# Kernel optimization log

Hardware: AMD Instinct MI355X
Metric: run time of the kernel (lower is better)

The kernel has to match this reference:

```python
import jax, jax.numpy as jnp
import numpy as np

B, S, D, H = 2, 2048, 2048, 16
DH = D // H  # 128
MAX_SEQ = 2048


def _rope_tables(dim, max_seq_len):
    inv_freq = 1.0 / (10000.0 ** (jnp.arange(0, dim, 2, dtype=jnp.float32) / dim))
    t = jnp.arange(max_seq_len, dtype=jnp.float32)
    freqs = jnp.einsum('i,j->ij', t, inv_freq)          # [S, dim/2]
    emb = jnp.concatenate([freqs, freqs], axis=-1)       # [S, dim]
    return jnp.cos(emb), jnp.sin(emb)


def setup_inputs() -> dict:
    key = jax.random.key(0)
    kx, kq, kk, kv, ko = jax.random.split(key, 5)
    scale = 1.0 / np.sqrt(D)
    x = jax.random.normal(kx, (B, S, D), dtype=jnp.float32)
    # nn.Linear weights: [out_features, in_features], y = x @ W.T
    wq = jax.random.normal(kq, (H * DH, D), dtype=jnp.float32) * scale
    wk = jax.random.normal(kk, (H * DH, D), dtype=jnp.float32) * scale
    wv = jax.random.normal(kv, (H * DH, D), dtype=jnp.float32) * scale
    wo = jax.random.normal(ko, (D, H * DH), dtype=jnp.float32) * scale
    cos, sin = _rope_tables(DH, MAX_SEQ)
    return {"x": x, "wq": wq, "wk": wk, "wv": wv, "wo": wo,
            "cos": cos, "sin": sin}


def _rotate(t):
    # faithful to torch: cat([-t[..., 1::2], t[..., ::2]], dim=-1)
    return jnp.concatenate([-t[..., 1::2], t[..., ::2]], axis=-1)


def reference(x, wq, wk, wv, wo, cos, sin):
    b, s, _ = x.shape
    # QKV projections -> [b, h, s, dh]
    def proj(w):
        return jnp.einsum('bsd,ed->bse', x, w).reshape(b, s, H, DH).transpose(0, 2, 1, 3)
    q, k, v = proj(wq), proj(wk), proj(wv)
    c = cos[:s, :]  # [s, dh], broadcasts over b, h
    si = sin[:s, :]
    q = q * c + _rotate(q) * si
    k = k * c + _rotate(k) * si
    # scaled dot-product attention, non-causal
    scores = jnp.einsum('bhqd,bhkd->bhqk', q, k) / np.sqrt(DH)
    attn = jax.nn.softmax(scores, axis=-1)
    out = jnp.einsum('bhqk,bhkd->bhqd', attn, v)
    out = out.transpose(0, 2, 1, 3).reshape(b, s, H * DH)
    return jnp.einsum('bse,de->bsd', out, wo)
```

## Files before the change

### kernel.cpp

```cpp
#include <hip/hip_runtime.h>

#define SQ   2048
#define DIMD 2048
#define NH   16
#define HD   128
#define MR   4096
#define QBLK 128
#define KBLK 64

using u16 = unsigned short;
using u32 = unsigned int;
using s16x8 = __attribute__((ext_vector_type(8))) short;
using u16x8 = __attribute__((ext_vector_type(8))) unsigned short;
using f32x4 = __attribute__((ext_vector_type(4))) float;
using as3u  = __attribute__((address_space(3))) u32;
using as1u  = __attribute__((address_space(1))) u32;

__device__ __forceinline__ u16 f2bf(float f) {
  u32 x = __float_as_uint(f);
  return (u16)((x + 0x7fffu + ((x >> 16) & 1u)) >> 16);
}
__device__ __forceinline__ float bf2f(u16 u) {
  return __uint_as_float(((u32)u) << 16);
}
__device__ __forceinline__ void gld16(const void* g, void* l) {
  __builtin_amdgcn_global_load_lds((as1u*)g, (as3u*)l, 16, 0, 0);
}
#define MFMA16 __builtin_amdgcn_mfma_f32_16x16x32_bf16

__global__ __launch_bounds__(256) void cvt_bf16(const float* __restrict__ s,
                                                u16* __restrict__ d, int n4) {
  int i = blockIdx.x * 256 + threadIdx.x;
  int st = gridDim.x * 256;
  for (; i < n4; i += st) {
    float4 v = ((const float4*)s)[i];
    u32 lo = (u32)f2bf(v.x) | ((u32)f2bf(v.y) << 16);
    u32 hi = (u32)f2bf(v.z) | ((u32)f2bf(v.w) << 16);
    ((uint2*)d)[i] = make_uint2(lo, hi);
  }
}

__global__ __launch_bounds__(256) void cvt_w4(const float* __restrict__ w0,
                                              const float* __restrict__ w1,
                                              const float* __restrict__ w2,
                                              const float* __restrict__ w3,
                                              u16* __restrict__ d) {
  const int n4 = DIMD * DIMD / 4;
  int y = blockIdx.y;
  const float* s = (y == 0) ? w0 : (y == 1) ? w1 : (y == 2) ? w2 : w3;
  u16* dst = d + (size_t)y * DIMD * DIMD;
  int i = blockIdx.x * 256 + threadIdx.x;
  int st = gridDim.x * 256;
  for (; i < n4; i += st) {
    float4 v = ((const float4*)s)[i];
    u32 lo = (u32)f2bf(v.x) | ((u32)f2bf(v.y) << 16);
    u32 hi = (u32)f2bf(v.z) | ((u32)f2bf(v.w) << 16);
    ((uint2*)dst)[i] = make_uint2(lo, hi);
  }
}

__global__ __launch_bounds__(256) void rope_kernel(
    const u16* __restrict__ Qin, const u16* __restrict__ Kin,
    u16* __restrict__ Qout, u16* __restrict__ Kout,
    const float* __restrict__ cosT, const float* __restrict__ sinT) {
  int ten = blockIdx.y;
  const u16* in = ten ? Kin : Qin;
  u16* outp     = ten ? Kout : Qout;
  float scl     = ten ? 1.0f : 0.08838834764831845f;
  int row = blockIdx.x * 4 + (threadIdx.x >> 6);
  int j   = threadIdx.x & 63;
  int s   = row & (SQ - 1);
  const u16* r = in + (size_t)row * HD;
  u16* w = outp + (size_t)row * HD;
  float c  = cosT[s * HD + j];
  float si = sinT[s * HD + j];
  float a  = bf2f(r[j]);
  float b  = bf2f(r[j + 64]);
  float ev = bf2f(r[2 * j]);
  float od = bf2f(r[2 * j + 1]);
  w[j]      = f2bf((a * c - od * si) * scl);
  w[j + 64] = f2bf((b * c + ev * si) * scl);
}

__global__ __launch_bounds__(256) void transpose_v(const u16* __restrict__ V,
                                                   u16* __restrict__ Vt) {
  __shared__ u16 tile[64][72];
  int sb = blockIdx.x, db = blockIdx.y, bh = blockIdx.z;
  int r  = threadIdx.x >> 3;
  int c8 = (threadIdx.x & 7) * 8;
  const u16* src = V + ((size_t)bh * SQ + sb * 64) * HD + db * 64;
#pragma unroll
  for (int p2 = 0; p2 < 2; p2++) {
    int row = p2 * 32 + r;
    u16x8 v = *(const u16x8*)(src + (size_t)row * HD + c8);
#pragma unroll
    for (int k2 = 0; k2 < 8; k2++) tile[row][c8 + k2] = v[k2];
  }
  __syncthreads();
  u16* dst = Vt + ((size_t)bh * HD + db * 64) * SQ + sb * 64;
#pragma unroll
  for (int p2 = 0; p2 < 2; p2++) {
    int dr = p2 * 32 + r;
    u16x8 o;
#pragma unroll
    for (int k2 = 0; k2 < 8; k2++) o[k2] = tile[c8 + k2][dr];
    *(u16x8*)(dst + (size_t)dr * SQ + c8) = o;
  }
}

template <int MODE>
__global__ __launch_bounds__(256) void gemm_bt(
    const u16* __restrict__ A,
    const u16* __restrict__ W0, const u16* __restrict__ W1, const u16* __restrict__ W2,
    u16* __restrict__ O0, u16* __restrict__ O1, u16* __restrict__ O2,
    float* __restrict__ Ofp) {
  __shared__ alignas(16) u16 lA[2][128 * 32];
  __shared__ alignas(16) u16 lB[2][128 * 32];
  int t = threadIdx.x;
  int l = t & 63, l15 = l & 15, lg = l >> 4;
  int wid = t >> 6, wr = wid >> 1, wc = wid & 1;
  int mi = blockIdx.x >> 4, ni = blockIdx.x & 15;
  int m0 = mi * 128, n0 = ni * 128;
  const u16* W = W0;
  u16* Ob = O0;
  if (MODE == 0) {
    if (blockIdx.y == 1) { W = W1; Ob = O1; }
    else if (blockIdx.y == 2) { W = W2; Ob = O2; }
  }
  const u16* Ag = A + (size_t)m0 * DIMD;
  const u16* Wg = W + (size_t)n0 * DIMD;
  int r0 = t >> 2, ch = (t & 3) * 8;

  f32x4 acc[4][4];
#pragma unroll
  for (int a1 = 0; a1 < 4; a1++)
#pragma unroll
    for (int b1 = 0; b1 < 4; b1++) acc[a1][b1] = (f32x4){0.f, 0.f, 0.f, 0.f};

  auto stage = [&](int buf, int kb) {
    int k0 = kb * 32;
    gld16(Ag + (size_t)r0 * DIMD + k0 + ch,        &lA[buf][t * 8]);
    gld16(Ag + (size_t)(r0 + 64) * DIMD + k0 + ch, &lA[buf][(t + 256) * 8]);
    gld16(Wg + (size_t)r0 * DIMD + k0 + ch,        &lB[buf][t * 8]);
    gld16(Wg + (size_t)(r0 + 64) * DIMD + k0 + ch, &lB[buf][(t + 256) * 8]);
  };

  stage(0, 0);
  __syncthreads();
#pragma unroll 2
  for (int kb = 0; kb < DIMD / 32; kb++) {
    if (kb + 1 < DIMD / 32) stage((kb + 1) & 1, kb + 1);
    int buf = kb & 1;
    s16x8 af[4], bfr[4];
#pragma unroll
    for (int rb = 0; rb < 4; rb++)
      af[rb] = *(const s16x8*)&lA[buf][(wr * 64 + rb * 16 + l15) * 32 + lg * 8];
#pragma unroll
    for (int cb = 0; cb < 4; cb++)
      bfr[cb] = *(const s16x8*)&lB[buf][(wc * 64 + cb * 16 + l15) * 32 + lg * 8];
#pragma unroll
    for (int rb = 0; rb < 4; rb++)
#pragma unroll
      for (int cb = 0; cb < 4; cb++)
        acc[rb][cb] = MFMA16(af[rb], bfr[cb], acc[rb][cb], 0, 0, 0);
    __syncthreads();
  }
#pragma unroll
  for (int rb = 0; rb < 4; rb++) {
#pragma unroll
    for (int cb = 0; cb < 4; cb++) {
#pragma unroll
      for (int i = 0; i < 4; i++) {
        float v = acc[rb][cb][i];
        int mm = m0 + wr * 64 + rb * 16 + lg * 4 + i;
        int nn = n0 + wc * 64 + cb * 16 + l15;
        if (MODE == 0) {
          int b = mm >> 11, s2 = mm & (SQ - 1), h = nn >> 7, dh = nn & (HD - 1);
          Ob[((size_t)(b * NH + h) * SQ + s2) * HD + dh] = f2bf(v);
        } else {
          Ofp[(size_t)mm * DIMD + nn] = v;
        }
      }
    }
  }
}

__global__ __launch_bounds__(512, 4) void attn_kernel(
    const u16* __restrict__ Q, const u16* __restrict__ K,
    const u16* __restrict__ Vt, u16* __restrict__ Aout) {
  __shared__ alignas(16) u16 Ksh[2][KBLK * HD];
  __shared__ alignas(16) u16 Vsh[2][HD * KBLK];
  __shared__ alignas(16) u16 Pl[8][16 * KBLK];
  int t = threadIdx.x;
  int wid = t >> 6, l = t & 63, l15 = l & 15, lg = l >> 4;
  int orig = blockIdx.x;
  int bid = (orig & 7) * 64 + (orig >> 3);
  int qb = bid & 15, bh = bid >> 4;
  int q0 = qb * QBLK + wid * 16;
  const u16* Qb = Q + ((size_t)bh * SQ + q0) * HD;
  const u16* Kb = K + (size_t)bh * SQ * HD;
  const u16* Vb = Vt + (size_t)bh * HD * SQ;

  s16x8 qf[4];
#pragma unroll
  for (int ks = 0; ks < 4; ks++)
    qf[ks] = *(const s16x8*)(Qb + (size_t)l15 * HD + ks * 32 + lg * 8);

  int o0 = t * 16, o1 = t * 16 + 8192;
  int kr0 = o0 >> 8, kc0 = (o0 & 255) ^ ((kr0 & 7) << 4);
  int kr1 = o1 >> 8, kc1 = (o1 & 255) ^ ((kr1 & 7) << 4);
  int vr0 = o0 >> 7, vc0 = (o0 & 127) ^ ((vr0 & 7) << 4);
  int vr1 = o1 >> 7, vc1 = (o1 & 127) ^ ((vr1 & 7) << 4);

  auto stage = [&](int buf, int kb) {
    const u16* Kt = Kb + (size_t)kb * KBLK * HD;
    const u16* Vs = Vb + kb * KBLK;
    gld16(Kt + (size_t)kr0 * HD + (kc0 >> 1), &Ksh[buf][o0 >> 1]);
    gld16(Kt + (size_t)kr1 * HD + (kc1 >> 1), &Ksh[buf][o1 >> 1]);
    gld16(Vs + (size_t)vr0 * SQ + (vc0 >> 1), &Vsh[buf][o0 >> 1]);
    gld16(Vs + (size_t)vr1 * SQ + (vc1 >> 1), &Vsh[buf][o1 >> 1]);
  };

  f32x4 acc[8];
#pragma unroll
  for (int i = 0; i < 8; i++) acc[i] = (f32x4){0.f, 0.f, 0.f, 0.f};
  float m = -3.0e38f, lsum = 0.f;

  stage(0, 0);
  __syncthreads();

#pragma unroll 1
  for (int kb = 0; kb < SQ / KBLK; kb++) {
    int cur = kb & 1;
    if (kb + 1 < SQ / KBLK) stage(cur ^ 1, kb + 1);
    f32x4 sa[4];
#pragma unroll
    for (int cb = 0; cb < 4; cb++) sa[cb] = (f32x4){0.f, 0.f, 0.f, 0.f};
    __builtin_amdgcn_s_setprio(1);
#pragma unroll
    for (int ks = 0; ks < 4; ks++) {
#pragma unroll
      for (int cb = 0; cb < 4; cb++) {
        int r = cb * 16 + l15;
        int off = r * 256 + ((ks * 64 + lg * 16) ^ ((r & 7) << 4));
        s16x8 kf = *(const s16x8*)((const char*)&Ksh[cur][0] + off);
        sa[cb] = MFMA16(kf, qf[ks], sa[cb], 0, 0, 0);
      }
    }
    __builtin_amdgcn_s_setprio(0);
    float rm = sa[0][0];
#pragma unroll
    for (int cb = 0; cb < 4; cb++)
#pragma unroll
      for (int i = 0; i < 4; i++) rm = fmaxf(rm, sa[cb][i]);
    rm = fmaxf(rm, __shfl_xor(rm, 16));
    rm = fmaxf(rm, __shfl_xor(rm, 32));
    if (!__all(rm <= m + 8.0f)) {
      float mn = fmaxf(m, rm);
      float al = __expf(m - mn);
      m = mn;
      float alq[4];
#pragma unroll
      for (int i = 0; i < 4; i++) alq[i] = __shfl(al, lg * 4 + i, 16);
#pragma unroll
      for (int c2 = 0; c2 < 8; c2++)
#pragma unroll
        for (int i = 0; i < 4; i++) acc[c2][i] *= alq[i];
      lsum *= al;
    }
    float ps = 0.f;
#pragma unroll
    for (int cb = 0; cb < 4; cb++)
#pragma unroll
      for (int i = 0; i < 4; i++) {
        sa[cb][i] = __expf(sa[cb][i] - m);
        ps += sa[cb][i];
      }
    ps += __shfl_xor(ps, 16);
    ps += __shfl_xor(ps, 32);
    lsum += ps;
#pragma unroll
    for (int cb = 0; cb < 4; cb++) {
      u32 lo = (u32)f2bf(sa[cb][0]) | ((u32)f2bf(sa[cb][1]) << 16);
      u32 hi = (u32)f2bf(sa[cb][2]) | ((u32)f2bf(sa[cb][3]) << 16);
      int off = l15 * 128 + ((cb * 32 + lg * 8) ^ ((l15 & 7) << 4));
      *(uint2*)((char*)&Pl[wid][0] + off) = make_uint2(lo, hi);
    }
    s16x8 pf[2];
#pragma unroll
    for (int k2 = 0; k2 < 2; k2++) {
      int off = l15 * 128 + ((k2 * 64 + lg * 16) ^ ((l15 & 7) << 4));
      pf[k2] = *(const s16x8*)((const char*)&Pl[wid][0] + off);
    }
    __builtin_amdgcn_s_setprio(1);
#pragma unroll
    for (int c2 = 0; c2 < 8; c2++) {
#pragma unroll
      for (int k2 = 0; k2 < 2; k2++) {
        int r = c2 * 16 + l15;
        int off = r * 128 + ((k2 * 64 + lg * 16) ^ ((r & 7) << 4));
        s16x8 vf = *(const s16x8*)((const char*)&Vsh[cur][0] + off);
        acc[c2] = MFMA16(pf[k2], vf, acc[c2], 0, 0, 0);
      }
    }
    __builtin_amdgcn_s_setprio(0);
    __syncthreads();
  }
  float rin = 1.0f / lsum;
  float rq[4];
#pragma unroll
  for (int i = 0; i < 4; i++) rq[i] = __shfl(rin, lg * 4 + i, 16);
  int b = bh >> 4, h = bh & (NH - 1);
#pragma unroll
  for (int c2 = 0; c2 < 8; c2++) {
#pragma unroll
    for (int i = 0; i < 4; i++) {
      int q = q0 + lg * 4 + i;
      int dh = c2 * 16 + l15;
      Aout[((size_t)b * SQ + q) * DIMD + h * HD + dh] = f2bf(acc[c2][i] * rq[i]);
    }
  }
}

extern "C" void kernel_launch(void* const* d_in, const int* in_sizes, int n_in,
                              void* d_out, int out_size, void* d_ws, size_t ws_size,
                              hipStream_t stream) {
  (void)in_sizes; (void)n_in; (void)out_size; (void)ws_size;
  const float* x    = (const float*)d_in[0];
  const float* wq   = (const float*)d_in[1];
  const float* wk   = (const float*)d_in[2];
  const float* wv   = (const float*)d_in[3];
  const float* wo   = (const float*)d_in[4];
  const float* cosT = (const float*)d_in[5];
  const float* sinT = (const float*)d_in[6];
  float* out = (float*)d_out;

  char* p = (char*)d_ws;
  const size_t SZ_MD = (size_t)MR * DIMD * 2;
  const size_t SZ_W  = (size_t)DIMD * DIMD * 2;
  u16* xb   = (u16*)p; p += SZ_MD;
  u16* wqb  = (u16*)p; p += SZ_W;
  u16* wkb  = (u16*)p; p += SZ_W;
  u16* wvb  = (u16*)p; p += SZ_W;
  u16* wob  = (u16*)p; p += SZ_W;
  u16* Qraw = (u16*)p; p += SZ_MD;
  u16* Kraw = (u16*)p; p += SZ_MD;
  u16* Qr   = (u16*)p; p += SZ_MD;
  u16* Kr   = (u16*)p; p += SZ_MD;
  u16* Vraw = (u16*)p; p += SZ_MD;
  u16* Vt   = (u16*)p; p += SZ_MD;
  u16* attnout = Qraw;

  cvt_bf16<<<1024, 256, 0, stream>>>(x, xb, MR * DIMD / 4);
  cvt_w4<<<dim3(512, 4), 256, 0, stream>>>(wq, wk, wv, wo, wqb);

  gemm_bt<0><<<dim3(512, 3), 256, 0, stream>>>(xb, wqb, wkb, wvb, Qraw, Kraw, Vraw, nullptr);
  rope_kernel<<<dim3(16384, 2), 256, 0, stream>>>(Qraw, Kraw, Qr, Kr, cosT, sinT);
  transpose_v<<<dim3(32, 2, 32), 256, 0, stream>>>(Vraw, Vt);
  attn_kernel<<<512, 512, 0, stream>>>(Qr, Kr, Vt, attnout);
  gemm_bt<1><<<dim3(512, 1), 256, 0, stream>>>(attnout, wob, nullptr, nullptr,
                                               nullptr, nullptr, nullptr, out);
}
```

Measured before the change: 322.0 us.

## Fuse V transpose into QKV GEMM epilogue and widen attention warps to 32 rows

The QKV GEMM now writes V already transposed, staging the tile through padded shared memory in its epilogue, so the separate transpose_v kernel and its extra round trip through memory are gone. The attention kernel moves to 256-thread blocks where each wave handles 32 query rows (two 16-row MFMA tiles) instead of 16. Each K/V fragment read from LDS is therefore reused across twice as many MFMAs. The cost is higher register pressure and lower occupancy in attention, plus a strided transposed store in the GEMM epilogue.

```diff
diff --git a/kernel.cpp b/kernel.cpp
--- a/kernel.cpp
+++ b/kernel.cpp
@@ -82,40 +82,15 @@
   w[j + 64] = f2bf((b * c + ev * si) * scl);
 }
 
-__global__ __launch_bounds__(256) void transpose_v(const u16* __restrict__ V,
-                                                   u16* __restrict__ Vt) {
-  __shared__ u16 tile[64][72];
-  int sb = blockIdx.x, db = blockIdx.y, bh = blockIdx.z;
-  int r  = threadIdx.x >> 3;
-  int c8 = (threadIdx.x & 7) * 8;
-  const u16* src = V + ((size_t)bh * SQ + sb * 64) * HD + db * 64;
-#pragma unroll
-  for (int p2 = 0; p2 < 2; p2++) {
-    int row = p2 * 32 + r;
-    u16x8 v = *(const u16x8*)(src + (size_t)row * HD + c8);
-#pragma unroll
-    for (int k2 = 0; k2 < 8; k2++) tile[row][c8 + k2] = v[k2];
-  }
-  __syncthreads();
-  u16* dst = Vt + ((size_t)bh * HD + db * 64) * SQ + sb * 64;
-#pragma unroll
-  for (int p2 = 0; p2 < 2; p2++) {
-    int dr = p2 * 32 + r;
-    u16x8 o;
-#pragma unroll
-    for (int k2 = 0; k2 < 8; k2++) o[k2] = tile[c8 + k2][dr];
-    *(u16x8*)(dst + (size_t)dr * SQ + c8) = o;
-  }
-}
-
 template <int MODE>
 __global__ __launch_bounds__(256) void gemm_bt(
     const u16* __restrict__ A,
     const u16* __restrict__ W0, const u16* __restrict__ W1, const u16* __restrict__ W2,
     u16* __restrict__ O0, u16* __restrict__ O1, u16* __restrict__ O2,
     float* __restrict__ Ofp) {
-  __shared__ alignas(16) u16 lA[2][128 * 32];
-  __shared__ alignas(16) u16 lB[2][128 * 32];
+  __shared__ alignas(16) u16 SM[17408];
+  u16* lA = SM;
+  u16* lB = SM + 8192;
   int t = threadIdx.x;
   int l = t & 63, l15 = l & 15, lg = l >> 4;
   int wid = t >> 6, wr = wid >> 1, wc = wid & 1;
@@ -139,10 +114,10 @@
 
   auto stage = [&](int buf, int kb) {
     int k0 = kb * 32;
-    gld16(Ag + (size_t)r0 * DIMD + k0 + ch,        &lA[buf][t * 8]);
-    gld16(Ag + (size_t)(r0 + 64) * DIMD + k0 + ch, &lA[buf][(t + 256) * 8]);
-    gld16(Wg + (size_t)r0 * DIMD + k0 + ch,        &lB[buf][t * 8]);
-    gld16(Wg + (size_t)(r0 + 64) * DIMD + k0 + ch, &lB[buf][(t + 256) * 8]);
+    gld16(Ag + (size_t)r0 * DIMD + k0 + ch,        &lA[buf * 4096 + t * 8]);
+    gld16(Ag + (size_t)(r0 + 64) * DIMD + k0 + ch, &lA[buf * 4096 + (t + 256) * 8]);
+    gld16(Wg + (size_t)r0 * DIMD + k0 + ch,        &lB[buf * 4096 + t * 8]);
+    gld16(Wg + (size_t)(r0 + 64) * DIMD + k0 + ch, &lB[buf * 4096 + (t + 256) * 8]);
   };
 
   stage(0, 0);
@@ -154,10 +129,10 @@
     s16x8 af[4], bfr[4];
 #pragma unroll
     for (int rb = 0; rb < 4; rb++)
-      af[rb] = *(const s16x8*)&lA[buf][(wr * 64 + rb * 16 + l15) * 32 + lg * 8];
+      af[rb] = *(const s16x8*)&lA[buf * 4096 + (wr * 64 + rb * 16 + l15) * 32 + lg * 8];
 #pragma unroll
     for (int cb = 0; cb < 4; cb++)
-      bfr[cb] = *(const s16x8*)&lB[buf][(wc * 64 + cb * 16 + l15) * 32 + lg * 8];
+      bfr[cb] = *(const s16x8*)&lB[buf * 4096 + (wc * 64 + cb * 16 + l15) * 32 + lg * 8];
 #pragma unroll
     for (int rb = 0; rb < 4; rb++)
 #pragma unroll
@@ -165,6 +140,31 @@
         acc[rb][cb] = MFMA16(af[rb], bfr[cb], acc[rb][cb], 0, 0, 0);
     __syncthreads();
   }
+
+  if (MODE == 0 && blockIdx.y == 2) {
+    u16 (*lT)[132] = (u16(*)[132])SM;
+#pragma unroll
+    for (int rb = 0; rb < 4; rb++)
+#pragma unroll
+      for (int cb = 0; cb < 4; cb++)
+#pragma unroll
+        for (int i = 0; i < 4; i++)
+          lT[wr * 64 + rb * 16 + lg * 4 + i][wc * 64 + cb * 16 + l15] =
+              f2bf(acc[rb][cb][i]);
+    __syncthreads();
+    int b = m0 >> 11, s0 = m0 & (SQ - 1), h = n0 >> 7;
+    int dh = t >> 1, sc = (t & 1) * 64;
+    u16* dst = Ob + ((size_t)(b * NH + h) * HD + dh) * SQ + s0 + sc;
+#pragma unroll
+    for (int c8 = 0; c8 < 8; c8++) {
+      u16x8 o;
+#pragma unroll
+      for (int e = 0; e < 8; e++) o[e] = lT[sc + c8 * 8 + e][dh];
+      *(u16x8*)(dst + c8 * 8) = o;
+    }
+    return;
+  }
+
 #pragma unroll
   for (int rb = 0; rb < 4; rb++) {
 #pragma unroll
@@ -185,46 +185,55 @@
   }
 }
 
-__global__ __launch_bounds__(512, 4) void attn_kernel(
+__global__ __launch_bounds__(256, 2) void attn_kernel(
     const u16* __restrict__ Q, const u16* __restrict__ K,
     const u16* __restrict__ Vt, u16* __restrict__ Aout) {
   __shared__ alignas(16) u16 Ksh[2][KBLK * HD];
   __shared__ alignas(16) u16 Vsh[2][HD * KBLK];
-  __shared__ alignas(16) u16 Pl[8][16 * KBLK];
+  __shared__ alignas(16) u16 Pl[4][32 * KBLK];
   int t = threadIdx.x;
   int wid = t >> 6, l = t & 63, l15 = l & 15, lg = l >> 4;
   int orig = blockIdx.x;
   int bid = (orig & 7) * 64 + (orig >> 3);
   int qb = bid & 15, bh = bid >> 4;
-  int q0 = qb * QBLK + wid * 16;
+  int q0 = qb * QBLK + wid * 32;
   const u16* Qb = Q + ((size_t)bh * SQ + q0) * HD;
   const u16* Kb = K + (size_t)bh * SQ * HD;
   const u16* Vb = Vt + (size_t)bh * HD * SQ;
 
-  s16x8 qf[4];
-#pragma unroll
-  for (int ks = 0; ks < 4; ks++)
-    qf[ks] = *(const s16x8*)(Qb + (size_t)l15 * HD + ks * 32 + lg * 8);
-
-  int o0 = t * 16, o1 = t * 16 + 8192;
-  int kr0 = o0 >> 8, kc0 = (o0 & 255) ^ ((kr0 & 7) << 4);
-  int kr1 = o1 >> 8, kc1 = (o1 & 255) ^ ((kr1 & 7) << 4);
-  int vr0 = o0 >> 7, vc0 = (o0 & 127) ^ ((vr0 & 7) << 4);
-  int vr1 = o1 >> 7, vc1 = (o1 & 127) ^ ((vr1 & 7) << 4);
+  s16x8 qf[2][4];
+#pragma unroll
+  for (int mq = 0; mq < 2; mq++)
+#pragma unroll
+    for (int ks = 0; ks < 4; ks++)
+      qf[mq][ks] = *(const s16x8*)(Qb + (size_t)(mq * 16 + l15) * HD + ks * 32 + lg * 8);
+
+  int od[4], kro[4], kco[4], vro[4], vco[4];
+#pragma unroll
+  for (int p2 = 0; p2 < 4; p2++) {
+    int off = t * 16 + p2 * 4096;
+    od[p2] = off;
+    kro[p2] = off >> 8; kco[p2] = (off & 255) ^ ((kro[p2] & 7) << 4);
+    vro[p2] = off >> 7; vco[p2] = (off & 127) ^ ((vro[p2] & 7) << 4);
+  }
 
   auto stage = [&](int buf, int kb) {
     const u16* Kt = Kb + (size_t)kb * KBLK * HD;
     const u16* Vs = Vb + kb * KBLK;
-    gld16(Kt + (size_t)kr0 * HD + (kc0 >> 1), &Ksh[buf][o0 >> 1]);
-    gld16(Kt + (size_t)kr1 * HD + (kc1 >> 1), &Ksh[buf][o1 >> 1]);
-    gld16(Vs + (size_t)vr0 * SQ + (vc0 >> 1), &Vsh[buf][o0 >> 1]);
-    gld16(Vs + (size_t)vr1 * SQ + (vc1 >> 1), &Vsh[buf][o1 >> 1]);
+#pragma unroll
+    for (int p2 = 0; p2 < 4; p2++)
+      gld16(Kt + (size_t)kro[p2] * HD + (kco[p2] >> 1), &Ksh[buf][od[p2] >> 1]);
+#pragma unroll
+    for (int p2 = 0; p2 < 4; p2++)
+      gld16(Vs + (size_t)vro[p2] * SQ + (vco[p2] >> 1), &Vsh[buf][od[p2] >> 1]);
   };
 
-  f32x4 acc[8];
-#pragma unroll
-  for (int i = 0; i < 8; i++) acc[i] = (f32x4){0.f, 0.f, 0.f, 0.f};
-  float m = -3.0e38f, lsum = 0.f;
+  f32x4 acc[2][8];
+#pragma unroll
+  for (int mq = 0; mq < 2; mq++)
+#pragma unroll
+    for (int i = 0; i < 8; i++) acc[mq][i] = (f32x4){0.f, 0.f, 0.f, 0.f};
+  float m[2] = {-3.0e38f, -3.0e38f}, lsum[2] = {0.f, 0.f};
 
   stage(0, 0);
   __syncthreads();
@@ -233,9 +242,11 @@
   for (int kb = 0; kb < SQ / KBLK; kb++) {
     int cur = kb & 1;
     if (kb + 1 < SQ / KBLK) stage(cur ^ 1, kb + 1);
-    f32x4 sa[4];
-#pragma unroll
-    for (int cb = 0; cb < 4; cb++) sa[cb] = (f32x4){0.f, 0.f, 0.f, 0.f};
+    f32x4 sa[2][4];
+#pragma unroll
+    for (int mq = 0; mq < 2; mq++)
+#pragma unroll
+      for (int cb = 0; cb < 4; cb++) sa[mq][cb] = (f32x4){0.f, 0.f, 0.f, 0.f};
     __builtin_amdgcn_s_setprio(1);
 #pragma unroll
     for (int ks = 0; ks < 4; ks++) {
@@ -244,54 +255,70 @@
         int r = cb * 16 + l15;
         int off = r * 256 + ((ks * 64 + lg * 16) ^ ((r & 7) << 4));
         s16x8 kf = *(const s16x8*)((const char*)&Ksh[cur][0] + off);
-        sa[cb] = MFMA16(kf, qf[ks], sa[cb], 0, 0, 0);
+        sa[0][cb] = MFMA16(kf, qf[0][ks], sa[0][cb], 0, 0, 0);
+        sa[1][cb] = MFMA16(kf, qf[1][ks], sa[1][cb], 0, 0, 0);
       }
     }
     __builtin_amdgcn_s_setprio(0);
-    float rm = sa[0][0];
-#pragma unroll
-    for (int cb = 0; cb < 4; cb++)
-#pragma unroll
-      for (int i = 0; i < 4; i++) rm = fmaxf(rm, sa[cb][i]);
-    rm = fmaxf(rm, __shfl_xor(rm, 16));
-    rm = fmaxf(rm, __shfl_xor(rm, 32));
-    if (!__all(rm <= m + 8.0f)) {
-      float mn = fmaxf(m, rm);
-      float al = __expf(m - mn);
-      m = mn;
-      float alq[4];
-#pragma unroll
-      for (int i = 0; i < 4; i++) alq[i] = __shfl(al, lg * 4 + i, 16);
-#pragma unroll
-      for (int c2 = 0; c2 < 8; c2++)
-#pragma unroll
-        for (int i = 0; i < 4; i++) acc[c2][i] *= alq[i];
-      lsum *= al;
-    }
-    float ps = 0.f;
-#pragma unroll
-    for (int cb = 0; cb < 4; cb++)
-#pragma unroll
-      for (int i = 0; i < 4; i++) {
-        sa[cb][i] = __expf(sa[cb][i] - m);
-        ps += sa[cb][i];
-      }
-    ps += __shfl_xor(ps, 16);
-    ps += __shfl_xor(ps, 32);
-    lsum += ps;
-#pragma unroll
-    for (int cb = 0; cb < 4; cb++) {
-      u32 lo = (u32)f2bf(sa[cb][0]) | ((u32)f2bf(sa[cb][1]) << 16);
-      u32 hi = (u32)f2bf(sa[cb][2]) | ((u32)f2bf(sa[cb][3]) << 16);
-      int off = l15 * 128 + ((cb * 32 + lg * 8) ^ ((l15 & 7) << 4));
-      *(uint2*)((char*)&Pl[wid][0] + off) = make_uint2(lo, hi);
-    }
-    s16x8 pf[2];
-#pragma unroll
-    for (int k2 = 0; k2 < 2; k2++) {
-      int off = l15 * 128 + ((k2 * 64 + lg * 16) ^ ((l15 & 7) << 4));
-      pf[k2] = *(const s16x8*)((const char*)&Pl[wid][0] + off);
-    }
+    float rm[2];
+#pragma unroll
+    for (int mq = 0; mq < 2; mq++) {
+      float r2 = sa[mq][0][0];
+#pragma unroll
+      for (int cb = 0; cb < 4; cb++)
+#pragma unroll
+        for (int i = 0; i < 4; i++) r2 = fmaxf(r2, sa[mq][cb][i]);
+      r2 = fmaxf(r2, __shfl_xor(r2, 16));
+      r2 = fmaxf(r2, __shfl_xor(r2, 32));
+      rm[mq] = r2;
+    }
+    if (!__all(rm[0] <= m[0] + 8.0f && rm[1] <= m[1] + 8.0f)) {
+#pragma unroll
+      for (int mq = 0; mq < 2; mq++) {
+        float mn = fmaxf(m[mq], rm[mq]);
+        float al = __expf(m[mq] - mn);
+        m[mq] = mn;
+        float alq[4];
+#pragma unroll
+        for (int i = 0; i < 4; i++) alq[i] = __shfl(al, lg * 4 + i, 16);
+#pragma unroll
+        for (int c2 = 0; c2 < 8; c2++)
+#pragma unroll
+          for (int i = 0; i < 4; i++) acc[mq][c2][i] *= alq[i];
+        lsum[mq] *= al;
+      }
+    }
+#pragma unroll
+    for (int mq = 0; mq < 2; mq++) {
+      float ps = 0.f;
+#pragma unroll
+      for (int cb = 0; cb < 4; cb++)
+#pragma unroll
+        for (int i = 0; i < 4; i++) {
+          sa[mq][cb][i] = __expf(sa[mq][cb][i] - m[mq]);
+          ps += sa[mq][cb][i];
+        }
+      ps += __shfl_xor(ps, 16);
+      ps += __shfl_xor(ps, 32);
+      lsum[mq] += ps;
+    }
+#pragma unroll
+    for (int mq = 0; mq < 2; mq++)
+#pragma unroll
+      for (int cb = 0; cb < 4; cb++) {
+        u32 lo = (u32)f2bf(sa[mq][cb][0]) | ((u32)f2bf(sa[mq][cb][1]) << 16);
+        u32 hi = (u32)f2bf(sa[mq][cb][2]) | ((u32)f2bf(sa[mq][cb][3]) << 16);
+        int off = (mq * 16 + l15) * 128 + ((cb * 32 + lg * 8) ^ ((l15 & 7) << 4));
+        *(uint2*)((char*)&Pl[wid][0] + off) = make_uint2(lo, hi);
+      }
+    s16x8 pf[2][2];
+#pragma unroll
+    for (int mq = 0; mq < 2; mq++)
+#pragma unroll
+      for (int k2 = 0; k2 < 2; k2++) {
+        int off = (mq * 16 + l15) * 128 + ((k2 * 64 + lg * 16) ^ ((l15 & 7) << 4));
+        pf[mq][k2] = *(const s16x8*)((const char*)&Pl[wid][0] + off);
+      }
     __builtin_amdgcn_s_setprio(1);
 #pragma unroll
     for (int c2 = 0; c2 < 8; c2++) {
@@ -300,24 +327,28 @@
         int r = c2 * 16 + l15;
         int off = r * 128 + ((k2 * 64 + lg * 16) ^ ((r & 7) << 4));
         s16x8 vf = *(const s16x8*)((const char*)&Vsh[cur][0] + off);
-        acc[c2] = MFMA16(pf[k2], vf, acc[c2], 0, 0, 0);
+        acc[0][c2] = MFMA16(pf[0][k2], vf, acc[0][c2], 0, 0, 0);
+        acc[1][c2] = MFMA16(pf[1][k2], vf, acc[1][c2], 0, 0, 0);
       }
     }
     __builtin_amdgcn_s_setprio(0);
     __syncthreads();
   }
-  float rin = 1.0f / lsum;
-  float rq[4];
-#pragma unroll
-  for (int i = 0; i < 4; i++) rq[i] = __shfl(rin, lg * 4 + i, 16);
   int b = bh >> 4, h = bh & (NH - 1);
 #pragma unroll
-  for (int c2 = 0; c2 < 8; c2++) {
-#pragma unroll
-    for (int i = 0; i < 4; i++) {
-      int q = q0 + lg * 4 + i;
-      int dh = c2 * 16 + l15;
-      Aout[((size_t)b * SQ + q) * DIMD + h * HD + dh] = f2bf(acc[c2][i] * rq[i]);
+  for (int mq = 0; mq < 2; mq++) {
+    float rin = 1.0f / lsum[mq];
+    float rq[4];
+#pragma unroll
+    for (int i = 0; i < 4; i++) rq[i] = __shfl(rin, lg * 4 + i, 16);
+#pragma unroll
+    for (int c2 = 0; c2 < 8; c2++) {
+#pragma unroll
+      for (int i = 0; i < 4; i++) {
+        int q = q0 + mq * 16 + lg * 4 + i;
+        int dh = c2 * 16 + l15;
+        Aout[((size_t)b * SQ + q) * DIMD + h * HD + dh] = f2bf(acc[mq][c2][i] * rq[i]);
+      }
     }
   }
 }
@@ -347,17 +378,15 @@
   u16* Kraw = (u16*)p; p += SZ_MD;
   u16* Qr   = (u16*)p; p += SZ_MD;
   u16* Kr   = (u16*)p; p += SZ_MD;
-  u16* Vraw = (u16*)p; p += SZ_MD;
   u16* Vt   = (u16*)p; p += SZ_MD;
   u16* attnout = Qraw;
 
   cvt_bf16<<<1024, 256, 0, stream>>>(x, xb, MR * DIMD / 4);
   cvt_w4<<<dim3(512, 4), 256, 0, stream>>>(wq, wk, wv, wo, wqb);
 
-  gemm_bt<0><<<dim3(512, 3), 256, 0, stream>>>(xb, wqb, wkb, wvb, Qraw, Kraw, Vraw, nullptr);
+  gemm_bt<0><<<dim3(512, 3), 256, 0, stream>>>(xb, wqb, wkb, wvb, Qraw, Kraw, Vt, nullptr);
   rope_kernel<<<dim3(16384, 2), 256, 0, stream>>>(Qraw, Kraw, Qr, Kr, cosT, sinT);
-  transpose_v<<<dim3(32, 2, 32), 256, 0, stream>>>(Vraw, Vt);
-  attn_kernel<<<512, 512, 0, stream>>>(Qr, Kr, Vt, attnout);
+  attn_kernel<<<512, 256, 0, stream>>>(Qr, Kr, Vt, attnout);
   gemm_bt<1><<<dim3(512, 1), 256, 0, stream>>>(attnout, wob, nullptr, nullptr,
                                                nullptr, nullptr, nullptr, out);
 }
```

Result: faster. 311.3 us (-3.3%).
